# Kernel tuning notes

Measured on AMD Instinct MI355X. Metric: run time of the kernel, lower is better.

## Reference

```python
import jax, jax.numpy as jnp
import numpy as np

BS, SEQ, C = 8, 1024, 1024

def setup_inputs() -> dict:
    key = jax.random.key(0)
    ks = jax.random.split(key, 5)
    inp = {
        "input": jax.random.normal(ks[0], (BS, SEQ, C), dtype=jnp.float32),
        "Wq": jax.random.normal(ks[1], (C, C), dtype=jnp.float32) * 0.001,
        "Wk": jax.random.normal(ks[2], (C, C), dtype=jnp.float32) * 0.001,
        "Wv": jax.random.normal(ks[3], (C, C), dtype=jnp.float32) * 0.001,
        "bq": jnp.zeros((C,), dtype=jnp.float32),
        "bk": jnp.zeros((C,), dtype=jnp.float32),
        "bv": jnp.zeros((C,), dtype=jnp.float32),
        "bias_position": jnp.ones((SEQ, SEQ), dtype=jnp.float32),
    }
    return inp

def reference(input, Wq, Wk, Wv, bq, bk, bv, bias_position):
    # Linear layers (torch nn.Linear: x @ W.T + b)
    q = input @ Wq.T + bq                      # (bs, seq, c)
    k = input @ Wk.T + bk                      # (bs, seq, c)
    v = input @ Wv.T + bv                      # (bs, seq, c)
    # AFT: out[b,t,c] = sum_s exp(k[b,s,c] + bias[t,s]) * v[b,s,c]
    #                 / sum_s exp(k[b,s,c] + bias[t,s])
    # Factor exp(k + bias) = exp(bias) * exp(k) -> two GEMM-like einsums,
    # avoiding the (seq, bs, seq, c) intermediate of the original.
    ek = jnp.exp(k)                            # (bs, seq, c)
    eb = jnp.exp(bias_position)                # (t, s)
    numerator = jnp.einsum('ts,bsc->btc', eb, ek * v)   # (bs, t, c)
    denominator = jnp.einsum('ts,bsc->btc', eb, ek)     # (bs, t, c)
    out = jax.nn.sigmoid(q) * (numerator / denominator)
    return out
```

## Files before the change

### kernel.cpp

```cpp
#include <hip/hip_runtime.h>

#define BSZ 8
#define SEQL 1024
#define CHN 1024
#define M1 (BSZ*SEQL)

typedef __attribute__((ext_vector_type(8))) short bf16x8;
typedef __attribute__((ext_vector_type(4))) float f32x4;
typedef __attribute__((ext_vector_type(4))) unsigned short us4;
typedef __attribute__((ext_vector_type(8))) unsigned short us8;

static __device__ __forceinline__ unsigned short f2bf(float f){
  unsigned int u = __float_as_uint(f);
  u += 0x7fffu + ((u >> 16) & 1u);
  return (unsigned short)(u >> 16);
}
static __device__ __forceinline__ float bf2f(unsigned short h){
  return __uint_as_float(((unsigned int)h) << 16);
}
static __device__ __forceinline__ void gload16(const void* g, void* l){
  __builtin_amdgcn_global_load_lds((const __attribute__((address_space(1))) void*)g,
                                   (__attribute__((address_space(3))) void*)l,
                                   16, 0, 0);
}
static __device__ __forceinline__ int swzc(int row, int chunk){
  return chunk ^ ((row >> 1) & 3);
}

__global__ void prep_kernel(const float* __restrict__ x, const float* __restrict__ wq,
                            const float* __restrict__ wk, const float* __restrict__ wv,
                            const float* __restrict__ bias,
                            unsigned short* __restrict__ xb, unsigned short* __restrict__ wqb,
                            unsigned short* __restrict__ wkb, unsigned short* __restrict__ wvb,
                            unsigned short* __restrict__ ebb)
{
  const int NX = M1 * CHN;
  const int NW = CHN * CHN;
  const int total4 = (NX + 3 * NW + SEQL * SEQL) >> 2;
  for (int i = blockIdx.x * blockDim.x + threadIdx.x; i < total4;
       i += gridDim.x * blockDim.x) {
    int e = i << 2;
    const float* src; unsigned short* dst; int off; bool ex = false;
    if (e < NX)               { src = x;    dst = xb;  off = e; }
    else if (e < NX + NW)     { src = wq;   dst = wqb; off = e - NX; }
    else if (e < NX + 2 * NW) { src = wk;   dst = wkb; off = e - (NX + NW); }
    else if (e < NX + 3 * NW) { src = wv;   dst = wvb; off = e - (NX + 2 * NW); }
    else                      { src = bias; dst = ebb; off = e - (NX + 3 * NW); ex = true; }
    float4 v = *reinterpret_cast<const float4*>(src + off);
    if (ex) { v.x = expf(v.x); v.y = expf(v.y); v.z = expf(v.z); v.w = expf(v.w); }
    us4 o; o.x = f2bf(v.x); o.y = f2bf(v.y); o.z = f2bf(v.z); o.w = f2bf(v.w);
    *reinterpret_cast<us4*>(dst + off) = o;
  }
}

__global__ __launch_bounds__(256) void gemm_q(
    const unsigned short* __restrict__ Xb, const unsigned short* __restrict__ Wq,
    const float* __restrict__ bq, unsigned short* __restrict__ Qb)
{
  __shared__ unsigned short lds[8192];
  const int tid = threadIdx.x;
  const int lane = tid & 63;
  const int wm = tid >> 7;
  const int wn = (tid >> 6) & 1;
  const int nwg = gridDim.x;
  const int lid = blockIdx.x;
  const int sid = (lid & 7) * (nwg >> 3) + (lid >> 3);
  const int m0 = (sid >> 3) * 128;
  const int n0 = (sid & 7) * 128;

  const int linA0 = tid * 16, linA1 = 4096 + tid * 16;
  const int rA0 = linA0 >> 6, cA0 = (linA0 >> 4) & 3;
  const int rA1 = linA1 >> 6, cA1 = (linA1 >> 4) & 3;
  const unsigned short* gA0 = Xb + (m0 + rA0) * CHN + swzc(rA0, cA0) * 8;
  const unsigned short* gA1 = Xb + (m0 + rA1) * CHN + swzc(rA1, cA1) * 8;
  const unsigned short* gB0 = Wq + (n0 + rA0) * CHN + swzc(rA0, cA0) * 8;
  const unsigned short* gB1 = Wq + (n0 + rA1) * CHN + swzc(rA1, cA1) * 8;
  unsigned short* lA0 = lds + (linA0 >> 1);
  unsigned short* lA1 = lds + (linA1 >> 1);
  unsigned short* lB0 = lds + 4096 + (linA0 >> 1);
  unsigned short* lB1 = lds + 4096 + (linA1 >> 1);

  int aOff[4], bOff[4];
#pragma unroll
  for (int mi = 0; mi < 4; mi++) {
    int r = wm * 64 + mi * 16 + (lane & 15);
    aOff[mi] = r * 32 + swzc(r, lane >> 4) * 8;
  }
#pragma unroll
  for (int ni = 0; ni < 4; ni++) {
    int r = wn * 64 + ni * 16 + (lane & 15);
    bOff[ni] = 4096 + r * 32 + swzc(r, lane >> 4) * 8;
  }

  f32x4 acc[4][4] = {};
  for (int kk = 0; kk < CHN; kk += 32) {
    gload16(gA0 + kk, lA0); gload16(gA1 + kk, lA1);
    gload16(gB0 + kk, lB0); gload16(gB1 + kk, lB1);
    __syncthreads();
    bf16x8 af[4], bf[4];
#pragma unroll
    for (int mi = 0; mi < 4; mi++) af[mi] = *reinterpret_cast<const bf16x8*>(lds + aOff[mi]);
#pragma unroll
    for (int ni = 0; ni < 4; ni++) bf[ni] = *reinterpret_cast<const bf16x8*>(lds + bOff[ni]);
#pragma unroll
    for (int ni = 0; ni < 4; ni++)
#pragma unroll
      for (int mi = 0; mi < 4; mi++)
        acc[mi][ni] = __builtin_amdgcn_mfma_f32_16x16x32_bf16(af[mi], bf[ni], acc[mi][ni], 0, 0, 0);
    __syncthreads();
  }

  const int rb = (lane >> 4) * 4;
  float bqv[4];
#pragma unroll
  for (int ni = 0; ni < 4; ni++) bqv[ni] = bq[n0 + wn * 64 + ni * 16 + (lane & 15)];
#pragma unroll
  for (int mi = 0; mi < 4; mi++)
#pragma unroll
    for (int ni = 0; ni < 4; ni++)
#pragma unroll
      for (int r = 0; r < 4; r++) {
        int mrow = m0 + wm * 64 + mi * 16 + rb + r;
        int col  = n0 + wn * 64 + ni * 16 + (lane & 15);
        Qb[mrow * CHN + col] = f2bf(acc[mi][ni][r] + bqv[ni]);
      }
}

__global__ __launch_bounds__(256) void gemm_kv(
    const unsigned short* __restrict__ Xb,
    const unsigned short* __restrict__ Wk, const unsigned short* __restrict__ Wv,
    const float* __restrict__ bk, const float* __restrict__ bv,
    unsigned short* __restrict__ EKT, unsigned short* __restrict__ EKVT)
{
  __shared__ unsigned short lds[8704];
  const int tid = threadIdx.x;
  const int lane = tid & 63;
  const int wm = tid >> 7;
  const int wn = (tid >> 6) & 1;
  const int nwg = gridDim.x;
  const int lid = blockIdx.x;
  const int sid = (lid & 7) * (nwg >> 3) + (lid >> 3);
  const int m0 = (sid >> 4) * 128;
  const int n0 = (sid & 15) * 64;

  const int linA0 = tid * 16, linA1 = 4096 + tid * 16;
  const int rA0 = linA0 >> 6, cA0 = (linA0 >> 4) & 3;
  const int rA1 = linA1 >> 6, cA1 = (linA1 >> 4) & 3;
  const unsigned short* gA0 = Xb + (m0 + rA0) * CHN + swzc(rA0, cA0) * 8;
  const unsigned short* gA1 = Xb + (m0 + rA1) * CHN + swzc(rA1, cA1) * 8;
  const int rB = tid >> 2, cB = tid & 3;
  const unsigned short* gBk = Wk + (n0 + rB) * CHN + swzc(rB, cB) * 8;
  const unsigned short* gBv = Wv + (n0 + rB) * CHN + swzc(rB, cB) * 8;
  unsigned short* lA0 = lds + (linA0 >> 1);
  unsigned short* lA1 = lds + (linA1 >> 1);
  unsigned short* lBk = lds + 4096 + tid * 8;
  unsigned short* lBv = lds + 6144 + tid * 8;

  int aOff[4], bOff[2];
#pragma unroll
  for (int mi = 0; mi < 4; mi++) {
    int r = wm * 64 + mi * 16 + (lane & 15);
    aOff[mi] = r * 32 + swzc(r, lane >> 4) * 8;
  }
#pragma unroll
  for (int ni = 0; ni < 2; ni++) {
    int r = wn * 32 + ni * 16 + (lane & 15);
    bOff[ni] = r * 32 + swzc(r, lane >> 4) * 8;
  }

  f32x4 acck[4][2] = {}, accv[4][2] = {};
  for (int kk = 0; kk < CHN; kk += 32) {
    gload16(gA0 + kk, lA0); gload16(gA1 + kk, lA1);
    gload16(gBk + kk, lBk); gload16(gBv + kk, lBv);
    __syncthreads();
    bf16x8 af[4];
#pragma unroll
    for (int mi = 0; mi < 4; mi++) af[mi] = *reinterpret_cast<const bf16x8*>(lds + aOff[mi]);
#pragma unroll
    for (int ni = 0; ni < 2; ni++) {
      bf16x8 bk_ = *reinterpret_cast<const bf16x8*>(lds + 4096 + bOff[ni]);
      bf16x8 bv_ = *reinterpret_cast<const bf16x8*>(lds + 6144 + bOff[ni]);
#pragma unroll
      for (int mi = 0; mi < 4; mi++) {
        acck[mi][ni] = __builtin_amdgcn_mfma_f32_16x16x32_bf16(af[mi], bk_, acck[mi][ni], 0, 0, 0);
        accv[mi][ni] = __builtin_amdgcn_mfma_f32_16x16x32_bf16(af[mi], bv_, accv[mi][ni], 0, 0, 0);
      }
    }
    __syncthreads();
  }

  const int bIdx = m0 >> 10;
  const int s0 = m0 & 1023;
  const int rb = (lane >> 4) * 4;
  float bkv[2], bvv[2];
#pragma unroll
  for (int ni = 0; ni < 2; ni++) {
    int c = n0 + wn * 32 + ni * 16 + (lane & 15);
    bkv[ni] = bk[c]; bvv[ni] = bv[c];
  }
#pragma unroll
  for (int mi = 0; mi < 4; mi++)
#pragma unroll
    for (int ni = 0; ni < 2; ni++)
#pragma unroll
      for (int r = 0; r < 4; r++) {
        float ekf = expf(acck[mi][ni][r] + bkv[ni]);
        acck[mi][ni][r] = ekf;
        accv[mi][ni][r] = ekf * (accv[mi][ni][r] + bvv[ni]);
      }
#pragma unroll
  for (int mi = 0; mi < 4; mi++)
#pragma unroll
    for (int ni = 0; ni < 2; ni++) {
      int nloc = wn * 32 + ni * 16 + (lane & 15);
#pragma unroll
      for (int r = 0; r < 4; r++)
        lds[nloc * 136 + wm * 64 + mi * 16 + rb + r] = f2bf(acck[mi][ni][r]);
    }
  __syncthreads();
#pragma unroll
  for (int it = 0; it < 4; it++) {
    int ch = it * 256 + tid;
    int nloc = ch >> 4, c8 = ch & 15;
    us8 v = *reinterpret_cast<const us8*>(lds + nloc * 136 + c8 * 8);
    *reinterpret_cast<us8*>(EKT + (bIdx * CHN + n0 + nloc) * SEQL + s0 + c8 * 8) = v;
  }
  __syncthreads();
#pragma unroll
  for (int mi = 0; mi < 4; mi++)
#pragma unroll
    for (int ni = 0; ni < 2; ni++) {
      int nloc = wn * 32 + ni * 16 + (lane & 15);
#pragma unroll
      for (int r = 0; r < 4; r++)
        lds[nloc * 136 + wm * 64 + mi * 16 + rb + r] = f2bf(accv[mi][ni][r]);
    }
  __syncthreads();
#pragma unroll
  for (int it = 0; it < 4; it++) {
    int ch = it * 256 + tid;
    int nloc = ch >> 4, c8 = ch & 15;
    us8 v = *reinterpret_cast<const us8*>(lds + nloc * 136 + c8 * 8);
    *reinterpret_cast<us8*>(EKVT + (bIdx * CHN + n0 + nloc) * SEQL + s0 + c8 * 8) = v;
  }
}

__global__ __launch_bounds__(256) void gemm_aft(
    const unsigned short* __restrict__ EB,
    const unsigned short* __restrict__ EKT, const unsigned short* __restrict__ EKVT,
    const unsigned short* __restrict__ Qb, float* __restrict__ out)
{
  __shared__ unsigned short lds[8192];
  const int tid = threadIdx.x;
  const int lane = tid & 63;
  const int wm = tid >> 7;
  const int wn = (tid >> 6) & 1;
  const int nwg = gridDim.x;
  const int lid = blockIdx.x;
  const int sid = (lid & 7) * (nwg >> 3) + (lid >> 3);
  const int t0 = (sid & 7) * 128;
  const int n0 = (sid >> 3) * 64;

  const int linA0 = tid * 16, linA1 = 4096 + tid * 16;
  const int rA0 = linA0 >> 6, cA0 = (linA0 >> 4) & 3;
  const int rA1 = linA1 >> 6, cA1 = (linA1 >> 4) & 3;
  const unsigned short* gA0 = EB + (t0 + rA0) * SEQL + swzc(rA0, cA0) * 8;
  const unsigned short* gA1 = EB + (t0 + rA1) * SEQL + swzc(rA1, cA1) * 8;
  const int rB = tid >> 2, cB = tid & 3;
  const unsigned short* gBd = EKT + (n0 + rB) * SEQL + swzc(rB, cB) * 8;
  const unsigned short* gBn = EKVT + (n0 + rB) * SEQL + swzc(rB, cB) * 8;
  unsigned short* lA0 = lds + (linA0 >> 1);
  unsigned short* lA1 = lds + (linA1 >> 1);
  unsigned short* lBd = lds + 4096 + tid * 8;
  unsigned short* lBn = lds + 6144 + tid * 8;

  int aOff[4], bOff[2];
#pragma unroll
  for (int mi = 0; mi < 4; mi++) {
    int r = wm * 64 + mi * 16 + (lane & 15);
    aOff[mi] = r * 32 + swzc(r, lane >> 4) * 8;
  }
#pragma unroll
  for (int ni = 0; ni < 2; ni++) {
    int r = wn * 32 + ni * 16 + (lane & 15);
    bOff[ni] = r * 32 + swzc(r, lane >> 4) * 8;
  }

  f32x4 accd[4][2] = {}, accn[4][2] = {};
  for (int kk = 0; kk < SEQL; kk += 32) {
    gload16(gA0 + kk, lA0); gload16(gA1 + kk, lA1);
    gload16(gBd + kk, lBd); gload16(gBn + kk, lBn);
    __syncthreads();
    bf16x8 af[4];
#pragma unroll
    for (int mi = 0; mi < 4; mi++) af[mi] = *reinterpret_cast<const bf16x8*>(lds + aOff[mi]);
#pragma unroll
    for (int ni = 0; ni < 2; ni++) {
      bf16x8 bd_ = *reinterpret_cast<const bf16x8*>(lds + 4096 + bOff[ni]);
      bf16x8 bn_ = *reinterpret_cast<const bf16x8*>(lds + 6144 + bOff[ni]);
#pragma unroll
      for (int mi = 0; mi < 4; mi++) {
        accd[mi][ni] = __builtin_amdgcn_mfma_f32_16x16x32_bf16(af[mi], bd_, accd[mi][ni], 0, 0, 0);
        accn[mi][ni] = __builtin_amdgcn_mfma_f32_16x16x32_bf16(af[mi], bn_, accn[mi][ni], 0, 0, 0);
      }
    }
    __syncthreads();
  }

  const int rb = (lane >> 4) * 4;
#pragma unroll
  for (int mi = 0; mi < 4; mi++)
#pragma unroll
    for (int ni = 0; ni < 2; ni++) {
      int nloc = wn * 32 + ni * 16 + (lane & 15);
      int n = n0 + nloc;
      int b = n >> 10, c = n & 1023;
#pragma unroll
      for (int r = 0; r < 4; r++) {
        int t = t0 + wm * 64 + mi * 16 + rb + r;
        float qv = bf2f(Qb[(b * SEQL + t) * CHN + c]);
        float sig = 1.0f / (1.0f + expf(-qv));
        out[(b * SEQL + t) * CHN + c] = sig * accn[mi][ni][r] / accd[mi][ni][r];
      }
    }
}

extern "C" void kernel_launch(void* const* d_in, const int* in_sizes, int n_in,
                              void* d_out, int out_size, void* d_ws, size_t ws_size,
                              hipStream_t stream) {
  (void)in_sizes; (void)n_in; (void)out_size; (void)ws_size;
  const float* x    = (const float*)d_in[0];
  const float* wq   = (const float*)d_in[1];
  const float* wk   = (const float*)d_in[2];
  const float* wv   = (const float*)d_in[3];
  const float* bq   = (const float*)d_in[4];
  const float* bk   = (const float*)d_in[5];
  const float* bv   = (const float*)d_in[6];
  const float* bias = (const float*)d_in[7];
  float* out = (float*)d_out;

  char* ws = (char*)d_ws;
  const size_t MB = 1024 * 1024;
  unsigned short* Xb   = (unsigned short*)(ws);
  unsigned short* Wqb  = (unsigned short*)(ws + 16 * MB);
  unsigned short* Wkb  = (unsigned short*)(ws + 18 * MB);
  unsigned short* Wvb  = (unsigned short*)(ws + 20 * MB);
  unsigned short* EBb  = (unsigned short*)(ws + 22 * MB);
  unsigned short* Qb   = (unsigned short*)(ws + 24 * MB);
  unsigned short* EKT  = (unsigned short*)(ws + 40 * MB);
  unsigned short* EKVT = (unsigned short*)(ws + 56 * MB);

  prep_kernel<<<2048, 256, 0, stream>>>(x, wq, wk, wv, bias, Xb, Wqb, Wkb, Wvb, EBb);
  gemm_q<<<512, 256, 0, stream>>>(Xb, Wqb, bq, Qb);
  gemm_kv<<<1024, 256, 0, stream>>>(Xb, Wkb, Wvb, bk, bv, EKT, EKVT);
  gemm_aft<<<1024, 256, 0, stream>>>(EBb, EKT, EKVT, Qb, out);
}
```

Measured before the change: 228.9 us.

## Fuse Q projection into KV GEMM and double the K-step to 64

Merges the separate Q-projection GEMM into the K/V GEMM kernel, so one load of each X tile feeds three weight tiles and three accumulator sets. Both the projection and the AFT GEMMs now stage 64-wide K slices with an 8-chunk XOR swizzle, halving the number of barrier-separated iterations. The cost is more LDS per block (40KB and 32KB), more accumulator registers, and possibly lower occupancy. It also drops one kernel launch and the repeated reads of X.

```diff
diff --git a/kernel.cpp b/kernel.cpp
--- a/kernel.cpp
+++ b/kernel.cpp
@@ -22,9 +22,6 @@
   __builtin_amdgcn_global_load_lds((const __attribute__((address_space(1))) void*)g,
                                    (__attribute__((address_space(3))) void*)l,
                                    16, 0, 0);
-}
-static __device__ __forceinline__ int swzc(int row, int chunk){
-  return chunk ^ ((row >> 1) & 3);
 }
 
 __global__ void prep_kernel(const float* __restrict__ x, const float* __restrict__ wq,
@@ -53,86 +50,16 @@
   }
 }
 
-__global__ __launch_bounds__(256) void gemm_q(
-    const unsigned short* __restrict__ Xb, const unsigned short* __restrict__ Wq,
-    const float* __restrict__ bq, unsigned short* __restrict__ Qb)
-{
-  __shared__ unsigned short lds[8192];
-  const int tid = threadIdx.x;
-  const int lane = tid & 63;
-  const int wm = tid >> 7;
-  const int wn = (tid >> 6) & 1;
-  const int nwg = gridDim.x;
-  const int lid = blockIdx.x;
-  const int sid = (lid & 7) * (nwg >> 3) + (lid >> 3);
-  const int m0 = (sid >> 3) * 128;
-  const int n0 = (sid & 7) * 128;
-
-  const int linA0 = tid * 16, linA1 = 4096 + tid * 16;
-  const int rA0 = linA0 >> 6, cA0 = (linA0 >> 4) & 3;
-  const int rA1 = linA1 >> 6, cA1 = (linA1 >> 4) & 3;
-  const unsigned short* gA0 = Xb + (m0 + rA0) * CHN + swzc(rA0, cA0) * 8;
-  const unsigned short* gA1 = Xb + (m0 + rA1) * CHN + swzc(rA1, cA1) * 8;
-  const unsigned short* gB0 = Wq + (n0 + rA0) * CHN + swzc(rA0, cA0) * 8;
-  const unsigned short* gB1 = Wq + (n0 + rA1) * CHN + swzc(rA1, cA1) * 8;
-  unsigned short* lA0 = lds + (linA0 >> 1);
-  unsigned short* lA1 = lds + (linA1 >> 1);
-  unsigned short* lB0 = lds + 4096 + (linA0 >> 1);
-  unsigned short* lB1 = lds + 4096 + (linA1 >> 1);
-
-  int aOff[4], bOff[4];
-#pragma unroll
-  for (int mi = 0; mi < 4; mi++) {
-    int r = wm * 64 + mi * 16 + (lane & 15);
-    aOff[mi] = r * 32 + swzc(r, lane >> 4) * 8;
-  }
-#pragma unroll
-  for (int ni = 0; ni < 4; ni++) {
-    int r = wn * 64 + ni * 16 + (lane & 15);
-    bOff[ni] = 4096 + r * 32 + swzc(r, lane >> 4) * 8;
-  }
-
-  f32x4 acc[4][4] = {};
-  for (int kk = 0; kk < CHN; kk += 32) {
-    gload16(gA0 + kk, lA0); gload16(gA1 + kk, lA1);
-    gload16(gB0 + kk, lB0); gload16(gB1 + kk, lB1);
-    __syncthreads();
-    bf16x8 af[4], bf[4];
-#pragma unroll
-    for (int mi = 0; mi < 4; mi++) af[mi] = *reinterpret_cast<const bf16x8*>(lds + aOff[mi]);
-#pragma unroll
-    for (int ni = 0; ni < 4; ni++) bf[ni] = *reinterpret_cast<const bf16x8*>(lds + bOff[ni]);
-#pragma unroll
-    for (int ni = 0; ni < 4; ni++)
-#pragma unroll
-      for (int mi = 0; mi < 4; mi++)
-        acc[mi][ni] = __builtin_amdgcn_mfma_f32_16x16x32_bf16(af[mi], bf[ni], acc[mi][ni], 0, 0, 0);
-    __syncthreads();
-  }
-
-  const int rb = (lane >> 4) * 4;
-  float bqv[4];
-#pragma unroll
-  for (int ni = 0; ni < 4; ni++) bqv[ni] = bq[n0 + wn * 64 + ni * 16 + (lane & 15)];
-#pragma unroll
-  for (int mi = 0; mi < 4; mi++)
-#pragma unroll
-    for (int ni = 0; ni < 4; ni++)
-#pragma unroll
-      for (int r = 0; r < 4; r++) {
-        int mrow = m0 + wm * 64 + mi * 16 + rb + r;
-        int col  = n0 + wn * 64 + ni * 16 + (lane & 15);
-        Qb[mrow * CHN + col] = f2bf(acc[mi][ni][r] + bqv[ni]);
-      }
-}
-
-__global__ __launch_bounds__(256) void gemm_kv(
+__global__ __launch_bounds__(256) void gemm_qkv(
     const unsigned short* __restrict__ Xb,
-    const unsigned short* __restrict__ Wk, const unsigned short* __restrict__ Wv,
-    const float* __restrict__ bk, const float* __restrict__ bv,
+    const unsigned short* __restrict__ Wq, const unsigned short* __restrict__ Wk,
+    const unsigned short* __restrict__ Wv,
+    const float* __restrict__ bq, const float* __restrict__ bk,
+    const float* __restrict__ bv,
+    unsigned short* __restrict__ Qb,
     unsigned short* __restrict__ EKT, unsigned short* __restrict__ EKVT)
 {
-  __shared__ unsigned short lds[8704];
+  __shared__ unsigned short lds[20480];
   const int tid = threadIdx.x;
   const int lane = tid & 63;
   const int wm = tid >> 7;
@@ -143,47 +70,73 @@
   const int m0 = (sid >> 4) * 128;
   const int n0 = (sid & 15) * 64;
 
-  const int linA0 = tid * 16, linA1 = 4096 + tid * 16;
-  const int rA0 = linA0 >> 6, cA0 = (linA0 >> 4) & 3;
-  const int rA1 = linA1 >> 6, cA1 = (linA1 >> 4) & 3;
-  const unsigned short* gA0 = Xb + (m0 + rA0) * CHN + swzc(rA0, cA0) * 8;
-  const unsigned short* gA1 = Xb + (m0 + rA1) * CHN + swzc(rA1, cA1) * 8;
-  const int rB = tid >> 2, cB = tid & 3;
-  const unsigned short* gBk = Wk + (n0 + rB) * CHN + swzc(rB, cB) * 8;
-  const unsigned short* gBv = Wv + (n0 + rB) * CHN + swzc(rB, cB) * 8;
-  unsigned short* lA0 = lds + (linA0 >> 1);
-  unsigned short* lA1 = lds + (linA1 >> 1);
-  unsigned short* lBk = lds + 4096 + tid * 8;
-  unsigned short* lBv = lds + 6144 + tid * 8;
-
-  int aOff[4], bOff[2];
+  const unsigned short* srcA[4]; unsigned short* dstA[4];
+#pragma unroll
+  for (int p = 0; p < 4; p++) {
+    int l = p * 4096 + tid * 16;
+    int row = l >> 7;
+    int lc = ((l >> 4) & 7) ^ (row & 7);
+    srcA[p] = Xb + (m0 + row) * CHN + lc * 8;
+    dstA[p] = lds + (l >> 1);
+  }
+  const unsigned short* Ws0 = Wq; const unsigned short* Ws1 = Wk; const unsigned short* Ws2 = Wv;
+  const unsigned short* srcB[3][2]; unsigned short* dstB[3][2];
+#pragma unroll
+  for (int w = 0; w < 3; w++) {
+    const unsigned short* W = (w == 0) ? Ws0 : (w == 1) ? Ws1 : Ws2;
+#pragma unroll
+    for (int p = 0; p < 2; p++) {
+      int l = p * 4096 + tid * 16;
+      int row = l >> 7;
+      int lc = ((l >> 4) & 7) ^ (row & 7);
+      srcB[w][p] = W + (n0 + row) * CHN + lc * 8;
+      dstB[w][p] = lds + 8192 + w * 4096 + (l >> 1);
+    }
+  }
+
+  int aOff[4][2], bOff[2][2];
 #pragma unroll
   for (int mi = 0; mi < 4; mi++) {
     int r = wm * 64 + mi * 16 + (lane & 15);
-    aOff[mi] = r * 32 + swzc(r, lane >> 4) * 8;
+#pragma unroll
+    for (int ks = 0; ks < 2; ks++)
+      aOff[mi][ks] = r * 64 + ((((ks << 2) + (lane >> 4)) ^ (r & 7)) << 3);
   }
 #pragma unroll
   for (int ni = 0; ni < 2; ni++) {
     int r = wn * 32 + ni * 16 + (lane & 15);
-    bOff[ni] = r * 32 + swzc(r, lane >> 4) * 8;
-  }
-
-  f32x4 acck[4][2] = {}, accv[4][2] = {};
-  for (int kk = 0; kk < CHN; kk += 32) {
-    gload16(gA0 + kk, lA0); gload16(gA1 + kk, lA1);
-    gload16(gBk + kk, lBk); gload16(gBv + kk, lBv);
+#pragma unroll
+    for (int ks = 0; ks < 2; ks++)
+      bOff[ni][ks] = r * 64 + ((((ks << 2) + (lane >> 4)) ^ (r & 7)) << 3);
+  }
+
+  f32x4 accq[4][2] = {}, acck[4][2] = {}, accv[4][2] = {};
+
+  for (int kk = 0; kk < CHN; kk += 64) {
+#pragma unroll
+    for (int p = 0; p < 4; p++) gload16(srcA[p] + kk, dstA[p]);
+#pragma unroll
+    for (int w = 0; w < 3; w++)
+#pragma unroll
+      for (int p = 0; p < 2; p++) gload16(srcB[w][p] + kk, dstB[w][p]);
     __syncthreads();
-    bf16x8 af[4];
-#pragma unroll
-    for (int mi = 0; mi < 4; mi++) af[mi] = *reinterpret_cast<const bf16x8*>(lds + aOff[mi]);
-#pragma unroll
-    for (int ni = 0; ni < 2; ni++) {
-      bf16x8 bk_ = *reinterpret_cast<const bf16x8*>(lds + 4096 + bOff[ni]);
-      bf16x8 bv_ = *reinterpret_cast<const bf16x8*>(lds + 6144 + bOff[ni]);
-#pragma unroll
-      for (int mi = 0; mi < 4; mi++) {
-        acck[mi][ni] = __builtin_amdgcn_mfma_f32_16x16x32_bf16(af[mi], bk_, acck[mi][ni], 0, 0, 0);
-        accv[mi][ni] = __builtin_amdgcn_mfma_f32_16x16x32_bf16(af[mi], bv_, accv[mi][ni], 0, 0, 0);
+#pragma unroll
+    for (int ks = 0; ks < 2; ks++) {
+      bf16x8 af[4];
+#pragma unroll
+      for (int mi = 0; mi < 4; mi++)
+        af[mi] = *reinterpret_cast<const bf16x8*>(lds + aOff[mi][ks]);
+#pragma unroll
+      for (int ni = 0; ni < 2; ni++) {
+        bf16x8 bq_ = *reinterpret_cast<const bf16x8*>(lds + 8192 + bOff[ni][ks]);
+        bf16x8 bk_ = *reinterpret_cast<const bf16x8*>(lds + 12288 + bOff[ni][ks]);
+        bf16x8 bv_ = *reinterpret_cast<const bf16x8*>(lds + 16384 + bOff[ni][ks]);
+#pragma unroll
+        for (int mi = 0; mi < 4; mi++) {
+          accq[mi][ni] = __builtin_amdgcn_mfma_f32_16x16x32_bf16(af[mi], bq_, accq[mi][ni], 0, 0, 0);
+          acck[mi][ni] = __builtin_amdgcn_mfma_f32_16x16x32_bf16(af[mi], bk_, acck[mi][ni], 0, 0, 0);
+          accv[mi][ni] = __builtin_amdgcn_mfma_f32_16x16x32_bf16(af[mi], bv_, accv[mi][ni], 0, 0, 0);
+        }
       }
     }
     __syncthreads();
@@ -192,22 +145,26 @@
   const int bIdx = m0 >> 10;
   const int s0 = m0 & 1023;
   const int rb = (lane >> 4) * 4;
-  float bkv[2], bvv[2];
+  float bqv[2], bkv[2], bvv[2];
 #pragma unroll
   for (int ni = 0; ni < 2; ni++) {
     int c = n0 + wn * 32 + ni * 16 + (lane & 15);
-    bkv[ni] = bk[c]; bvv[ni] = bv[c];
+    bqv[ni] = bq[c]; bkv[ni] = bk[c]; bvv[ni] = bv[c];
   }
 #pragma unroll
   for (int mi = 0; mi < 4; mi++)
 #pragma unroll
-    for (int ni = 0; ni < 2; ni++)
+    for (int ni = 0; ni < 2; ni++) {
+      int col = n0 + wn * 32 + ni * 16 + (lane & 15);
 #pragma unroll
       for (int r = 0; r < 4; r++) {
+        int mrow = m0 + wm * 64 + mi * 16 + rb + r;
+        Qb[mrow * CHN + col] = f2bf(accq[mi][ni][r] + bqv[ni]);
         float ekf = expf(acck[mi][ni][r] + bkv[ni]);
         acck[mi][ni][r] = ekf;
         accv[mi][ni][r] = ekf * (accv[mi][ni][r] + bvv[ni]);
       }
+    }
 #pragma unroll
   for (int mi = 0; mi < 4; mi++)
 #pragma unroll
@@ -250,7 +207,7 @@
     const unsigned short* __restrict__ EKT, const unsigned short* __restrict__ EKVT,
     const unsigned short* __restrict__ Qb, float* __restrict__ out)
 {
-  __shared__ unsigned short lds[8192];
+  __shared__ unsigned short lds[16384];
   const int tid = threadIdx.x;
   const int lane = tid & 63;
   const int wm = tid >> 7;
@@ -261,47 +218,70 @@
   const int t0 = (sid & 7) * 128;
   const int n0 = (sid >> 3) * 64;
 
-  const int linA0 = tid * 16, linA1 = 4096 + tid * 16;
-  const int rA0 = linA0 >> 6, cA0 = (linA0 >> 4) & 3;
-  const int rA1 = linA1 >> 6, cA1 = (linA1 >> 4) & 3;
-  const unsigned short* gA0 = EB + (t0 + rA0) * SEQL + swzc(rA0, cA0) * 8;
-  const unsigned short* gA1 = EB + (t0 + rA1) * SEQL + swzc(rA1, cA1) * 8;
-  const int rB = tid >> 2, cB = tid & 3;
-  const unsigned short* gBd = EKT + (n0 + rB) * SEQL + swzc(rB, cB) * 8;
-  const unsigned short* gBn = EKVT + (n0 + rB) * SEQL + swzc(rB, cB) * 8;
-  unsigned short* lA0 = lds + (linA0 >> 1);
-  unsigned short* lA1 = lds + (linA1 >> 1);
-  unsigned short* lBd = lds + 4096 + tid * 8;
-  unsigned short* lBn = lds + 6144 + tid * 8;
-
-  int aOff[4], bOff[2];
+  const unsigned short* srcA[4]; unsigned short* dstA[4];
+#pragma unroll
+  for (int p = 0; p < 4; p++) {
+    int l = p * 4096 + tid * 16;
+    int row = l >> 7;
+    int lc = ((l >> 4) & 7) ^ (row & 7);
+    srcA[p] = EB + (t0 + row) * SEQL + lc * 8;
+    dstA[p] = lds + (l >> 1);
+  }
+  const unsigned short* srcB[2][2]; unsigned short* dstB[2][2];
+#pragma unroll
+  for (int w = 0; w < 2; w++) {
+    const unsigned short* B = (w == 0) ? EKT : EKVT;
+#pragma unroll
+    for (int p = 0; p < 2; p++) {
+      int l = p * 4096 + tid * 16;
+      int row = l >> 7;
+      int lc = ((l >> 4) & 7) ^ (row & 7);
+      srcB[w][p] = B + (n0 + row) * SEQL + lc * 8;
+      dstB[w][p] = lds + 8192 + w * 4096 + (l >> 1);
+    }
+  }
+
+  int aOff[4][2], bOff[2][2];
 #pragma unroll
   for (int mi = 0; mi < 4; mi++) {
     int r = wm * 64 + mi * 16 + (lane & 15);
-    aOff[mi] = r * 32 + swzc(r, lane >> 4) * 8;
+#pragma unroll
+    for (int ks = 0; ks < 2; ks++)
+      aOff[mi][ks] = r * 64 + ((((ks << 2) + (lane >> 4)) ^ (r & 7)) << 3);
   }
 #pragma unroll
   for (int ni = 0; ni < 2; ni++) {
     int r = wn * 32 + ni * 16 + (lane & 15);
-    bOff[ni] = r * 32 + swzc(r, lane >> 4) * 8;
+#pragma unroll
+    for (int ks = 0; ks < 2; ks++)
+      bOff[ni][ks] = r * 64 + ((((ks << 2) + (lane >> 4)) ^ (r & 7)) << 3);
   }
 
   f32x4 accd[4][2] = {}, accn[4][2] = {};
-  for (int kk = 0; kk < SEQL; kk += 32) {
-    gload16(gA0 + kk, lA0); gload16(gA1 + kk, lA1);
-    gload16(gBd + kk, lBd); gload16(gBn + kk, lBn);
+
+  for (int kk = 0; kk < SEQL; kk += 64) {
+#pragma unroll
+    for (int p = 0; p < 4; p++) gload16(srcA[p] + kk, dstA[p]);
+#pragma unroll
+    for (int w = 0; w < 2; w++)
+#pragma unroll
+      for (int p = 0; p < 2; p++) gload16(srcB[w][p] + kk, dstB[w][p]);
     __syncthreads();
-    bf16x8 af[4];
-#pragma unroll
-    for (int mi = 0; mi < 4; mi++) af[mi] = *reinterpret_cast<const bf16x8*>(lds + aOff[mi]);
-#pragma unroll
-    for (int ni = 0; ni < 2; ni++) {
-      bf16x8 bd_ = *reinterpret_cast<const bf16x8*>(lds + 4096 + bOff[ni]);
-      bf16x8 bn_ = *reinterpret_cast<const bf16x8*>(lds + 6144 + bOff[ni]);
-#pragma unroll
-      for (int mi = 0; mi < 4; mi++) {
-        accd[mi][ni] = __builtin_amdgcn_mfma_f32_16x16x32_bf16(af[mi], bd_, accd[mi][ni], 0, 0, 0);
-        accn[mi][ni] = __builtin_amdgcn_mfma_f32_16x16x32_bf16(af[mi], bn_, accn[mi][ni], 0, 0, 0);
+#pragma unroll
+    for (int ks = 0; ks < 2; ks++) {
+      bf16x8 af[4];
+#pragma unroll
+      for (int mi = 0; mi < 4; mi++)
+        af[mi] = *reinterpret_cast<const bf16x8*>(lds + aOff[mi][ks]);
+#pragma unroll
+      for (int ni = 0; ni < 2; ni++) {
+        bf16x8 bd_ = *reinterpret_cast<const bf16x8*>(lds + 8192 + bOff[ni][ks]);
+        bf16x8 bn_ = *reinterpret_cast<const bf16x8*>(lds + 12288 + bOff[ni][ks]);
+#pragma unroll
+        for (int mi = 0; mi < 4; mi++) {
+          accd[mi][ni] = __builtin_amdgcn_mfma_f32_16x16x32_bf16(af[mi], bd_, accd[mi][ni], 0, 0, 0);
+          accn[mi][ni] = __builtin_amdgcn_mfma_f32_16x16x32_bf16(af[mi], bn_, accn[mi][ni], 0, 0, 0);
+        }
       }
     }
     __syncthreads();
@@ -351,7 +331,6 @@
   unsigned short* EKVT = (unsigned short*)(ws + 56 * MB);
 
   prep_kernel<<<2048, 256, 0, stream>>>(x, wq, wk, wv, bias, Xb, Wqb, Wkb, Wvb, EBb);
-  gemm_q<<<512, 256, 0, stream>>>(Xb, Wqb, bq, Qb);
-  gemm_kv<<<1024, 256, 0, stream>>>(Xb, Wkb, Wvb, bk, bv, EKT, EKVT);
+  gemm_qkv<<<1024, 256, 0, stream>>>(Xb, Wqb, Wkb, Wvb, bq, bk, bv, Qb, EKT, EKVT);
   gemm_aft<<<1024, 256, 0, stream>>>(EBb, EKT, EKVT, Qb, out);
 }
```

Result: faster. 202.7 us (-11.5%).
